# Optimization experiments

Hardware: AMD Instinct MI355X
Metric: run time of the kernel (lower is better)

Reference implementation:

```python
import jax, jax.numpy as jnp
import numpy as np

B, T, D = 4, 4096, 1024
H, KP = 16, 256  # heads, low-rank seq projection dim
DK = D // H


def setup_inputs() -> dict:
    key = jax.random.key(0)
    ks = jax.random.split(key, 8)
    s = 1.0 / np.sqrt(D)
    xav = np.sqrt(6.0 / (T + KP))  # xavier_uniform for (max_seq_len, k_proj_dim)
    return {
        "x": jax.random.normal(ks[0], (B, T, D), jnp.float32),
        "Wq": jax.random.normal(ks[1], (D, D), jnp.float32) * s,
        "Wk": jax.random.normal(ks[2], (D, D), jnp.float32) * s,
        "Wv": jax.random.normal(ks[3], (D, D), jnp.float32) * s,
        "Ek": jax.random.uniform(ks[4], (T, KP), jnp.float32, -xav, xav),
        "Ev": jax.random.uniform(ks[5], (T, KP), jnp.float32, -xav, xav),
        "Wo": jax.random.normal(ks[6], (D, D), jnp.float32) * s,
        "bo": jnp.zeros((D,), jnp.float32),
    }


def reference(x, Wq, Wk, Wv, Ek, Ev, Wo, bo):
    Bx, Tx, _ = x.shape
    # QKV projections -> (B, H, T, DK)
    def split_heads(y):
        return y.reshape(Bx, Tx, H, DK).transpose(0, 2, 1, 3)
    Q = split_heads(x @ Wq)
    K = split_heads(x @ Wk)
    V = split_heads(x @ Wv)
    # Low-rank projection along sequence length: T -> KP
    K_proj = jnp.einsum('bhtd,tk->bhkd', K, Ek[:Tx])
    V_proj = jnp.einsum('bhtd,tk->bhkd', V, Ev[:Tx])
    scale = 1.0 / np.sqrt(DK)
    scores = jnp.einsum('bhtd,bhkd->bhtk', Q, K_proj) * scale
    attn = jax.nn.softmax(scores, axis=-1)
    ctx = jnp.einsum('bhtk,bhkd->bhtd', attn, V_proj)
    out = ctx.transpose(0, 2, 1, 3).reshape(Bx, Tx, D)
    return out @ Wo + bo  # dropout p=0.0 (eval) -> identity
```

## Files before the change

### kernel.cpp

```cpp
#include <hip/hip_runtime.h>

typedef unsigned short u16;
typedef __attribute__((ext_vector_type(8))) short short8;
typedef __attribute__((ext_vector_type(4))) float f32x4;

#define T_SEQ 4096
#define DMODEL 1024
#define NH 16
#define DKH 64
#define KPROJ 256

__device__ __forceinline__ u16 f2bf(float f) {
  union { float f; unsigned u; } v; v.f = f;
  unsigned r = v.u + 0x7FFFu + ((v.u >> 16) & 1u);
  return (u16)(r >> 16);
}
__device__ __forceinline__ float bf2f(u16 h) {
  union { unsigned u; float f; } v; v.u = ((unsigned)h) << 16; return v.f;
}
__device__ __forceinline__ unsigned cvt_pk_bf16(float a, float b) {
  unsigned r;
  asm("v_cvt_pk_bf16_f32 %0, %1, %2" : "=v"(r) : "v"(a), "v"(b));
  return r;
}

__device__ __forceinline__ void gl2lds16(const u16* g, u16* l) {
  __builtin_amdgcn_global_load_lds(
      (const __attribute__((address_space(1))) unsigned int*)g,
      (__attribute__((address_space(3))) unsigned int*)(unsigned int)(unsigned long long)l,
      16, 0, 0);
}

__global__ void sniff_dtype(const u16* __restrict__ x, int* __restrict__ flag) {
  int c = 0;
  for (int i = threadIdx.x; i < 8192; i += 64)
    if ((x[2 * i] & 0x7F80) == 0x7F80) c++;
#pragma unroll
  for (int m = 1; m < 64; m <<= 1) c += __shfl_xor(c, m);
  if (threadIdx.x == 0) *flag = (c > 0) ? 1 : 0;
}

__global__ void transpose_x(const void* __restrict__ in, u16* __restrict__ outT,
                            u16* __restrict__ outR, const int* __restrict__ flag) {
  __shared__ u16 tile[32][33];
  const bool f32 = (*flag != 0);
  const size_t zoff = (size_t)blockIdx.z * T_SEQ * DMODEL;
  const int c0 = blockIdx.x * 32, r0 = blockIdx.y * 32;
  for (int i = threadIdx.y; i < 32; i += 8) {
    const size_t idx = zoff + (size_t)(r0 + i) * DMODEL + c0 + threadIdx.x;
    const u16 v = f32 ? f2bf(((const float*)in)[idx]) : ((const u16*)in)[idx];
    tile[i][threadIdx.x] = v;
    outR[idx] = v;
  }
  __syncthreads();
  for (int i = threadIdx.y; i < 32; i += 8)
    outT[zoff + (size_t)(c0 + i) * T_SEQ + r0 + threadIdx.x] = tile[threadIdx.x][i];
}

__global__ void transpose_cvt4(const void* __restrict__ p0, const void* __restrict__ p1,
                               const void* __restrict__ p2, const void* __restrict__ p3,
                               u16* __restrict__ out, int R, int C, const int* __restrict__ flag) {
  __shared__ u16 tile[32][33];
  const bool f32 = (*flag != 0);
  const int z = blockIdx.z;
  const void* in = (z == 0) ? p0 : (z == 1) ? p1 : (z == 2) ? p2 : p3;
  const size_t zoff = (size_t)z * R * C;
  const int c0 = blockIdx.x * 32, r0 = blockIdx.y * 32;
  for (int i = threadIdx.y; i < 32; i += 8) {
    const size_t idx = (size_t)(r0 + i) * C + c0 + threadIdx.x;
    tile[i][threadIdx.x] = f32 ? f2bf(((const float*)in)[idx]) : ((const u16*)in)[idx];
  }
  __syncthreads();
  for (int i = threadIdx.y; i < 32; i += 8)
    out[zoff + (size_t)(c0 + i) * R + r0 + threadIdx.x] = tile[threadIdx.x][i];
}

__global__ void reduce_splitk(const float* __restrict__ P, u16* __restrict__ out) {
  const int b = blockIdx.y;
  const int j = (blockIdx.x * 256 + threadIdx.x) * 8;
  const float* p = P + (size_t)b * 4 * 524288 + j;
  float acc[8] = {};
#pragma unroll
  for (int s = 0; s < 4; ++s) {
    const float4 v0 = *(const float4*)(p + (size_t)s * 524288);
    const float4 v1 = *(const float4*)(p + (size_t)s * 524288 + 4);
    acc[0] += v0.x; acc[1] += v0.y; acc[2] += v0.z; acc[3] += v0.w;
    acc[4] += v1.x; acc[5] += v1.y; acc[6] += v1.z; acc[7] += v1.w;
  }
  union { u16 s[8]; short8 v; } o;
#pragma unroll
  for (int k = 0; k < 8; ++k) o.s[k] = f2bf(acc[k]);
  *(short8*)(out + (size_t)b * 524288 + j) = o.v;
}

template <int MODE>
__global__ void __launch_bounds__(256) gemm_bt(const u16* __restrict__ A0, const u16* __restrict__ Bt0,
                                               const void* __restrict__ bias, void* __restrict__ Cv,
                                               const int* __restrict__ flag, int M, int N, int K,
                                               int ldA, int ldB, size_t sA, size_t sB, size_t sC) {
  __shared__ __align__(16) u16 As[3][128 * 32];
  __shared__ __align__(16) u16 Bs[3][128 * 32];

  const int gx = gridDim.x, gy = gridDim.y;
  const int gxy = gx * gy;
  const int nwg = gxy * gridDim.z;
  int lin = (blockIdx.z * gy + blockIdx.y) * gx + blockIdx.x;
  if ((nwg & 7) == 0) lin = (lin & 7) * (nwg >> 3) + (lin >> 3);
  const int bz = lin / gxy;
  const int rem = lin - bz * gxy;
  const int by = rem / gx;
  const int bx = rem - by * gx;

  const int z = bz;
  const int bb = (MODE == 2) ? (z >> 2) : z;
  const int kstart = (MODE == 2) ? ((z & 3) * K) : 0;
  const u16* A = A0 + (size_t)bb * sA;
  const u16* Bt = Bt0 + (size_t)bb * sB;
  const int tid = threadIdx.x;
  const int wid = tid >> 6, lane = tid & 63;
  const int wm = wid >> 1, wn = wid & 1;
  const int quad = lane >> 4, l16 = lane & 15;
  const int m0 = by * 128, n0 = bx * 128;

  const int srow = lane >> 2;
  const int scol = (((lane & 3) ^ ((lane >> 3) & 3)) * 8);

  const u16* Ag = A + (size_t)(m0 + srow) * ldA + scol + kstart;
  const u16* Bg = Bt + (size_t)(n0 + srow) * ldB + scol + kstart;

  f32x4 acc[4][4] = {};

  auto stage = [&](int buf, int k0) {
#pragma unroll
    for (int r = 0; r < 2; ++r) {
      const int rowb = r * 64 + wid * 16;
      gl2lds16(Ag + (size_t)rowb * ldA + k0, &As[buf][rowb * 32]);
      gl2lds16(Bg + (size_t)rowb * ldB + k0, &Bs[buf][rowb * 32]);
    }
  };

  const int nI = K >> 5;
  stage(0, 0);
  stage(1, 32);

  const int rslot = (quad ^ ((l16 >> 1) & 3)) * 8;

  int cur = 0;
  for (int t = 0; t < nI; ++t) {
    if (t + 1 < nI) {
      asm volatile("s_waitcnt lgkmcnt(0) vmcnt(4)" ::: "memory");
    } else {
      asm volatile("s_waitcnt lgkmcnt(0) vmcnt(0)" ::: "memory");
    }
    __builtin_amdgcn_sched_barrier(0);
    __builtin_amdgcn_s_barrier();
    __builtin_amdgcn_sched_barrier(0);

    const int nxt = (cur + 2 >= 3) ? (cur - 1) : (cur + 2);
    if (t + 2 < nI) stage(nxt, (t + 2) << 5);

    short8 a[4], b[4];
#pragma unroll
    for (int mi = 0; mi < 4; ++mi)
      a[mi] = *(const short8*)(&As[cur][(wm * 64 + mi * 16 + l16) * 32 + rslot]);
#pragma unroll
    for (int ni = 0; ni < 4; ++ni)
      b[ni] = *(const short8*)(&Bs[cur][(wn * 64 + ni * 16 + l16) * 32 + rslot]);
    __builtin_amdgcn_s_setprio(1);
#pragma unroll
    for (int mi = 0; mi < 4; ++mi)
#pragma unroll
      for (int ni = 0; ni < 4; ++ni)
        acc[mi][ni] = __builtin_amdgcn_mfma_f32_16x16x32_bf16(a[mi], b[ni], acc[mi][ni], 0, 0, 0);
    __builtin_amdgcn_s_setprio(0);

    cur = (cur + 1 >= 3) ? 0 : (cur + 1);
  }

  const bool f32out = (MODE == 1) && (*flag != 0);
  float* Pz = (MODE == 2) ? ((float*)Cv + (size_t)z * M * N) : nullptr;
#pragma unroll
  for (int mi = 0; mi < 4; ++mi) {
#pragma unroll
    for (int ni = 0; ni < 4; ++ni) {
      const int mloc = wm * 64 + mi * 16 + quad * 4;
      const int n = n0 + wn * 64 + ni * 16 + l16;
      float badd = 0.0f;
      if (MODE == 1)
        badd = f32out ? ((const float*)bias)[n] : bf2f(((const u16*)bias)[n]);
#pragma unroll
      for (int r = 0; r < 4; ++r) {
        if (MODE == 2) {
          Pz[(size_t)(m0 + mloc + r) * N + n] = acc[mi][ni][r];
        } else {
          const size_t oi = (size_t)bb * sC + (size_t)(m0 + mloc + r) * N + n;
          if (f32out) ((float*)Cv)[oi] = acc[mi][ni][r] + badd;
          else        ((u16*)Cv)[oi]  = f2bf(acc[mi][ni][r] + badd);
        }
      }
    }
  }
}

__global__ void __launch_bounds__(256, 2) attn_fused(const u16* Q, const u16* __restrict__ Kp,
                                                     const u16* __restrict__ VpT, u16* Ctx) {
  __shared__ __align__(16) u16 Ks[KPROJ * DKH];
  __shared__ __align__(16) u16 Vs[DKH * KPROJ];
  __shared__ __align__(16) u16 Ps[4 * 32 * 36];
  __shared__ __align__(16) float invS[4 * 32];

  int lin = blockIdx.y * gridDim.x + blockIdx.x;
  lin = (lin & 7) * 256 + (lin >> 3);
  const int bx = lin & 31;
  const int bh = lin >> 5;
  const int b = bh >> 4, h = bh & 15;
  const int tid = threadIdx.x, wid = tid >> 6, lane = tid & 63;
  const int quad = lane >> 4, l16 = lane & 15;
  const int t0 = bx * 128 + wid * 32;
  const u16* Qb = Q + ((size_t)b * T_SEQ + t0) * DMODEL + h * DKH;
  const u16* Kpb = Kp + (size_t)b * (KPROJ * DMODEL) + h * DKH;
  const u16* Vpb = VpT + (size_t)b * (DMODEL * KPROJ) + (size_t)(h * DKH) * KPROJ;
  u16* PsW = Ps + wid * (32 * 36);
  float* invW = invS + wid * 32;

  {
    const int srow = lane >> 3;
    const int scolb = ((lane & 7) * 16) ^ ((srow & 7) << 4);
#pragma unroll
    for (int i = 0; i < 8; ++i) {
      const int rbase = wid * 64 + i * 8;
      gl2lds16(Kpb + (size_t)(rbase + srow) * DMODEL + (scolb >> 1), Ks + rbase * DKH);
    }
    const int vrow = lane >> 5;
#pragma unroll
    for (int j = 0; j < 8; ++j) {
      const int dbase = wid * 16 + j * 2;
      const int d = dbase + vrow;
      const int vcolb = ((lane & 31) * 16) ^ ((d & 7) << 4);
      gl2lds16(Vpb + (size_t)d * KPROJ + (vcolb >> 1), Vs + dbase * KPROJ);
    }
  }

  short8 q[2][2];
#pragma unroll
  for (int kk = 0; kk < 2; ++kk) {
    q[kk][0] = *(const short8*)(Qb + (size_t)l16 * DMODEL + kk * 32 + quad * 8);
    q[kk][1] = *(const short8*)(Qb + (size_t)(16 + l16) * DMODEL + kk * 32 + quad * 8);
  }

  __syncthreads();

  f32x4 c0[4] = {}, c1[4] = {};
  float sm0 = 0.0f, sm1 = 0.0f;
  const float sc = 0.125f * 1.44269504f;

#pragma unroll
  for (int kt = 0; kt < 8; ++kt) {
    short8 kf[2][2];
#pragma unroll
    for (int m = 0; m < 2; ++m)
#pragma unroll
      for (int k2 = 0; k2 < 2; ++k2) {
        const int row = kt * 32 + m * 16 + l16;
        const int off = ((k2 * 64 + quad * 16) ^ ((row & 7) << 4)) >> 1;
        kf[m][k2] = *(const short8*)(Ks + row * DKH + off);
      }
    f32x4 st[2][2] = {};
    __builtin_amdgcn_s_setprio(1);
#pragma unroll
    for (int m = 0; m < 2; ++m)
#pragma unroll
      for (int k2 = 0; k2 < 2; ++k2) {
        st[m][0] = __builtin_amdgcn_mfma_f32_16x16x32_bf16(kf[m][k2], q[k2][0], st[m][0], 0, 0, 0);
        st[m][1] = __builtin_amdgcn_mfma_f32_16x16x32_bf16(kf[m][k2], q[k2][1], st[m][1], 0, 0, 0);
      }
    __builtin_amdgcn_s_setprio(0);

#pragma unroll
    for (int m = 0; m < 2; ++m) {
      const float a0 = exp2f(st[m][0][0] * sc), a1 = exp2f(st[m][0][1] * sc);
      const float a2 = exp2f(st[m][0][2] * sc), a3 = exp2f(st[m][0][3] * sc);
      const float b0 = exp2f(st[m][1][0] * sc), b1 = exp2f(st[m][1][1] * sc);
      const float b2 = exp2f(st[m][1][2] * sc), b3 = exp2f(st[m][1][3] * sc);
      sm0 += (a0 + a1) + (a2 + a3);
      sm1 += (b0 + b1) + (b2 + b3);
      *(uint2*)(PsW + l16 * 36 + m * 16 + quad * 4) =
          make_uint2(cvt_pk_bf16(a0, a1), cvt_pk_bf16(a2, a3));
      *(uint2*)(PsW + (16 + l16) * 36 + m * 16 + quad * 4) =
          make_uint2(cvt_pk_bf16(b0, b1), cvt_pk_bf16(b2, b3));
    }

    short8 vf[4];
#pragma unroll
    for (int ni = 0; ni < 4; ++ni) {
      const int d = ni * 16 + l16;
      const int off = ((kt * 64 + quad * 16) ^ ((d & 7) << 4)) >> 1;
      vf[ni] = *(const short8*)(Vs + d * KPROJ + off);
    }
    short8 pa0 = *(const short8*)(PsW + (size_t)l16 * 36 + quad * 8);
    short8 pa1 = *(const short8*)(PsW + (size_t)(16 + l16) * 36 + quad * 8);
    __builtin_amdgcn_s_setprio(1);
#pragma unroll
    for (int ni = 0; ni < 4; ++ni) {
      c0[ni] = __builtin_amdgcn_mfma_f32_16x16x32_bf16(pa0, vf[ni], c0[ni], 0, 0, 0);
      c1[ni] = __builtin_amdgcn_mfma_f32_16x16x32_bf16(pa1, vf[ni], c1[ni], 0, 0, 0);
    }
    __builtin_amdgcn_s_setprio(0);
  }

  sm0 += __shfl_xor(sm0, 16); sm0 += __shfl_xor(sm0, 32);
  sm1 += __shfl_xor(sm1, 16); sm1 += __shfl_xor(sm1, 32);
  if (quad == 0) {
    invW[l16] = 1.0f / sm0;
    invW[16 + l16] = 1.0f / sm1;
  }

  const float4 iv0 = *(const float4*)(invW + quad * 4);
  const float4 iv1 = *(const float4*)(invW + 16 + quad * 4);
  const float ivr0[4] = {iv0.x, iv0.y, iv0.z, iv0.w};
  const float ivr1[4] = {iv1.x, iv1.y, iv1.z, iv1.w};
#pragma unroll
  for (int ni = 0; ni < 4; ++ni)
#pragma unroll
    for (int r = 0; r < 4; ++r) {
      Ctx[((size_t)b * T_SEQ + t0 + quad * 4 + r) * DMODEL + h * DKH + ni * 16 + l16] =
          f2bf(c0[ni][r] * ivr0[r]);
      Ctx[((size_t)b * T_SEQ + t0 + 16 + quad * 4 + r) * DMODEL + h * DKH + ni * 16 + l16] =
          f2bf(c1[ni][r] * ivr1[r]);
    }
}

extern "C" void kernel_launch(void* const* d_in, const int* in_sizes, int n_in,
                              void* d_out, int out_size, void* d_ws, size_t ws_size,
                              hipStream_t stream) {
  (void)in_sizes; (void)n_in; (void)out_size; (void)ws_size;

  int* flag = (int*)d_ws;
  u16* base = (u16*)d_ws + 16;
  const size_t WSZ = 1048576;
  const size_t XSZ = 16777216;
  u16* wqT   = base + 0 * WSZ;
  u16* wkT   = base + 1 * WSZ;
  u16* wvT   = base + 2 * WSZ;
  u16* woT   = base + 3 * WSZ;
  u16* ekevT = base + 4 * WSZ;
  u16* xT    = base + 6 * WSZ;
  u16* xE    = xT + XSZ;
  u16* Kp    = xE + 4 * 524288;
  u16* VpT   = Kp + 4 * 262144;
  u16* Q     = VpT + 4 * 262144;
  u16* xbf   = (u16*)d_out;
  float* xEp = (float*)Q;

  sniff_dtype<<<1, 64, 0, stream>>>((const u16*)d_in[0], flag);

  dim3 tb(32, 8);
  transpose_x<<<dim3(32, 128, 4), tb, 0, stream>>>(d_in[0], xT, xbf, flag);
  transpose_cvt4<<<dim3(32, 32, 4), tb, 0, stream>>>(d_in[1], d_in[2], d_in[3], d_in[6],
                                                     wqT, 1024, 1024, flag);
  transpose_cvt4<<<dim3(8, 128, 2), tb, 0, stream>>>(d_in[4], d_in[5], nullptr, nullptr,
                                                     ekevT, 4096, 256, flag);

  gemm_bt<2><<<dim3(8, 4, 16), 256, 0, stream>>>(ekevT, xT, nullptr, xEp, flag,
                                                 512, 1024, 1024, 4096, 4096,
                                                 0, (size_t)DMODEL * T_SEQ, 0);
  reduce_splitk<<<dim3(256, 4), 256, 0, stream>>>(xEp, xE);

  gemm_bt<0><<<dim3(8, 2, 4), 256, 0, stream>>>(xE, wkT, nullptr, Kp, flag,
                                                256, 1024, 1024, 1024, 1024, 524288, 0, 262144);
  gemm_bt<0><<<dim3(2, 8, 4), 256, 0, stream>>>(wvT, xE + 262144, nullptr, VpT, flag,
                                                1024, 256, 1024, 1024, 1024, 0, 524288, 262144);
  gemm_bt<0><<<dim3(8, 128, 1), 256, 0, stream>>>(xbf, wqT, nullptr, Q, flag,
                                                  16384, 1024, 1024, 1024, 1024, 0, 0, 0);

  attn_fused<<<dim3(32, 64), 256, 0, stream>>>(Q, Kp, VpT, Q );

  gemm_bt<1><<<dim3(8, 128, 1), 256, 0, stream>>>(Q, woT, d_in[7], d_out, flag,
                                                  16384, 1024, 1024, 1024, 1024, 0, 0, 0);
}
```

Measured before the change: 417.3 us.

## Use 256x256-tile double-buffered GEMM kernel for Q and output projections

Adds a new GEMM kernel with 256x256 output tiles, 512 threads, and a double-buffered LDS pipeline that loads straight from global into LDS. It also applies an XOR swizzle to LDS slots and raises wave priority around the MFMA bursts. The two large 16384x1024x1024 projections (Q and the output) now use it in place of the 128-tile gemm_bt. The aim is more data reuse per tile and overlap of loads with compute. The cost is more registers per thread (128 accumulators) and fewer workgroups (256), which may leave some CUs idle or lower occupancy.

```diff
diff --git a/kernel.cpp b/kernel.cpp
--- a/kernel.cpp
+++ b/kernel.cpp
@@ -196,6 +196,107 @@
           const size_t oi = (size_t)bb * sC + (size_t)(m0 + mloc + r) * N + n;
           if (f32out) ((float*)Cv)[oi] = acc[mi][ni][r] + badd;
           else        ((u16*)Cv)[oi]  = f2bf(acc[mi][ni][r] + badd);
+        }
+      }
+    }
+  }
+}
+
+template <int MODE>
+__global__ void __launch_bounds__(512, 2) gemm256(const u16* __restrict__ A,
+                                                  const u16* __restrict__ Bt,
+                                                  const void* __restrict__ bias,
+                                                  void* __restrict__ Cv,
+                                                  const int* __restrict__ flag,
+                                                  int M, int N, int K) {
+  __shared__ __align__(16) u16 As[2][256 * 32];
+  __shared__ __align__(16) u16 Bs[2][256 * 32];
+
+  const int gx = gridDim.x;
+  const int nwg = gx * gridDim.y;
+  int lin = blockIdx.y * gx + blockIdx.x;
+  if ((nwg & 7) == 0) lin = (lin & 7) * (nwg >> 3) + (lin >> 3);
+  const int by = lin / gx;
+  const int bx = lin - by * gx;
+  const int m0 = by * 256, n0 = bx * 256;
+
+  const int tid = threadIdx.x;
+  const int wid = tid >> 6, lane = tid & 63;
+  const int wm = wid >> 2, wn = wid & 3;
+  const int quad = lane >> 4, l16 = lane & 15;
+
+  const int stR = wid * 16 + (lane >> 2);
+  const int sgs = ((lane & 3) ^ ((lane >> 3) & 3)) * 8;
+  const u16* AgS = A + (size_t)(m0 + stR) * K + sgs;
+  const u16* BgS = Bt + (size_t)(n0 + stR) * K + sgs;
+
+  auto stage = [&](int buf, int tk) {
+    const int kof = tk * 32;
+#pragma unroll
+    for (int e = 0; e < 2; ++e) {
+      const int rowb = e * 128 + wid * 16;
+      gl2lds16(AgS + (size_t)(e * 128) * K + kof, &As[buf][rowb * 32]);
+      gl2lds16(BgS + (size_t)(e * 128) * K + kof, &Bs[buf][rowb * 32]);
+    }
+  };
+
+  f32x4 acc[8][4] = {};
+  const int nT = K >> 5;
+
+  stage(0, 0);
+  stage(1, 1);
+
+  const int rslot = (quad ^ ((l16 >> 1) & 3)) * 8;
+
+  for (int t = 0; t < nT; ++t) {
+    const int cur = t & 1;
+    if (t + 1 < nT) {
+      asm volatile("s_waitcnt vmcnt(4)" ::: "memory");
+    } else {
+      asm volatile("s_waitcnt vmcnt(0)" ::: "memory");
+    }
+    __builtin_amdgcn_sched_barrier(0);
+    __builtin_amdgcn_s_barrier();
+    __builtin_amdgcn_sched_barrier(0);
+
+    short8 bf[4];
+#pragma unroll
+    for (int nf = 0; nf < 4; ++nf)
+      bf[nf] = *(const short8*)(&Bs[cur][(wn * 64 + nf * 16 + l16) * 32 + rslot]);
+#pragma unroll
+    for (int mf = 0; mf < 8; ++mf) {
+      const short8 af = *(const short8*)(&As[cur][(wm * 128 + mf * 16 + l16) * 32 + rslot]);
+      __builtin_amdgcn_s_setprio(1);
+#pragma unroll
+      for (int nf = 0; nf < 4; ++nf)
+        acc[mf][nf] = __builtin_amdgcn_mfma_f32_16x16x32_bf16(af, bf[nf], acc[mf][nf], 0, 0, 0);
+      __builtin_amdgcn_s_setprio(0);
+    }
+
+    asm volatile("s_waitcnt lgkmcnt(0)" ::: "memory");
+    __builtin_amdgcn_sched_barrier(0);
+    __builtin_amdgcn_s_barrier();
+    if (t + 2 < nT) stage(cur, t + 2);
+  }
+
+  const bool f32out = (MODE == 1) && (*flag != 0);
+#pragma unroll
+  for (int mf = 0; mf < 8; ++mf) {
+#pragma unroll
+    for (int nf = 0; nf < 4; ++nf) {
+      const int row = m0 + wm * 128 + mf * 16 + quad * 4;
+      const int col = n0 + wn * 64 + nf * 16 + l16;
+      float badd = 0.0f;
+      if (MODE == 1)
+        badd = f32out ? ((const float*)bias)[col] : bf2f(((const u16*)bias)[col]);
+#pragma unroll
+      for (int r = 0; r < 4; ++r) {
+        const size_t oi = (size_t)(row + r) * N + col;
+        if (MODE == 1) {
+          if (f32out) ((float*)Cv)[oi] = acc[mf][nf][r] + badd;
+          else        ((u16*)Cv)[oi]  = f2bf(acc[mf][nf][r] + badd);
+        } else {
+          ((u16*)Cv)[oi] = f2bf(acc[mf][nf][r]);
         }
       }
     }
@@ -370,11 +471,9 @@
                                                 256, 1024, 1024, 1024, 1024, 524288, 0, 262144);
   gemm_bt<0><<<dim3(2, 8, 4), 256, 0, stream>>>(wvT, xE + 262144, nullptr, VpT, flag,
                                                 1024, 256, 1024, 1024, 1024, 0, 524288, 262144);
-  gemm_bt<0><<<dim3(8, 128, 1), 256, 0, stream>>>(xbf, wqT, nullptr, Q, flag,
-                                                  16384, 1024, 1024, 1024, 1024, 0, 0, 0);
+  gemm256<0><<<dim3(4, 64), 512, 0, stream>>>(xbf, wqT, nullptr, Q, flag, 16384, 1024, 1024);
 
   attn_fused<<<dim3(32, 64), 256, 0, stream>>>(Q, Kp, VpT, Q );
 
-  gemm_bt<1><<<dim3(8, 128, 1), 256, 0, stream>>>(Q, woT, d_in[7], d_out, flag,
-                                                  16384, 1024, 1024, 1024, 1024, 0, 0, 0);
-}
+  gemm256<1><<<dim3(4, 64), 512, 0, stream>>>(Q, woT, d_in[7], d_out, flag, 16384, 1024, 1024);
+}
```

Result: faster. 395.6 us (-5.2%).
